# Performance work log

Hardware: AMD Instinct MI355X
Metric: run time of the kernel (lower is better)

Reference implementation:

```python
import jax, jax.numpy as jnp
import numpy as np

PATCH = 16

def setup_inputs() -> dict:
    key = jax.random.key(0)
    k1, k2, k3, k4, k5 = jax.random.split(key, 5)
    B, C, H, W = 128, 3, 224, 224
    N = (H // PATCH) * (W // PATCH)  # 196
    D = 768
    x = jax.random.normal(k1, (B, C, H, W), dtype=jnp.float32)
    ys = jax.random.randint(k2, (B, N), 0, H - PATCH + 1, dtype=jnp.int64)
    xs = jax.random.randint(k3, (B, N), 0, W - PATCH + 1, dtype=jnp.int64)
    W_proj = jax.random.normal(k4, (D, C * PATCH * PATCH), dtype=jnp.float32) * 0.02
    b_proj = jax.random.normal(k5, (D,), dtype=jnp.float32) * 0.02
    return {"x": x, "ys": ys, "xs": xs, "W_proj": W_proj, "b_proj": b_proj}

def reference(x, ys, xs, W_proj, b_proj):
    # x: [B, C, H, W]; ys, xs: [B, N] top-left patch coords
    B, C, H, W = x.shape
    N = ys.shape[1]
    P = PATCH
    # flattened within-patch offsets: d[p] = dy*W + dx, shape [P*P]
    dy = jnp.arange(P)[:, None]
    dx = jnp.arange(P)[None, :]
    d = (dy * W + dx).reshape(-1)  # [P*P]
    base = ys * W + xs                         # [B, N]
    indices = base[:, :, None] + d[None, None, :]  # [B, N, P*P]
    indices = indices.reshape(B, N * P * P)
    # gather over flattened spatial dims for every channel
    x_flat = x.reshape(B, C, H * W)
    patches = jnp.take_along_axis(
        x_flat, indices[:, None, :].astype(jnp.int32), axis=2
    )  # [B, C, N*P*P]
    patches = patches.reshape(B, C, N, P * P)
    patches = patches.transpose(0, 2, 1, 3).reshape(B, N, C * P * P)  # [B, N, C*P*P]
    patch_tokens = jnp.einsum('bnf,df->bnd', patches, W_proj) + b_proj  # [B, N, D]
    patch_positions = jnp.stack([ys, xs], axis=-1)  # [B, N, 2]
    return (patch_tokens, patch_positions)
```

## Files before the change

### kernel.cpp

```cpp
#include <hip/hip_runtime.h>
#include <hip/hip_bf16.h>

#define B_IMG   128
#define CH      3
#define HW      224
#define NPATCH  196
#define TOKENS  25088
#define PATCH   16
#define FDIM    768
#define DDIM    768
#define TOKELEMS ((size_t)TOKENS * FDIM)
#define OUT_TOKENS ((size_t)TOKENS * DDIM)

#define GATHER_BLOCKS (TOKENS * (FDIM / 4) / 256)
#define WCONV_BLOCKS  ((DDIM * FDIM / 4) / 256)

typedef short short8 __attribute__((ext_vector_type(8)));
typedef float f32x4  __attribute__((ext_vector_type(4)));

static __device__ __forceinline__ unsigned short f2bf(float v) {
  unsigned u = __float_as_uint(v);
  unsigned r = u + 0x7fffu + ((u >> 16) & 1u);
  return (unsigned short)(r >> 16);
}

static __device__ __forceinline__ void gload16(const short* g, short* l) {
  __builtin_amdgcn_global_load_lds(
      (const __attribute__((address_space(1))) void*)g,
      (__attribute__((address_space(3))) void*)l,
      16, 0, 0);
}

__global__ __launch_bounds__(256) void prep_kernel(
    const float* __restrict__ x, const int* __restrict__ ys,
    const int* __restrict__ xs, const float* __restrict__ W,
    short* __restrict__ patches, short* __restrict__ Wbf,
    float* __restrict__ pos) {
  const int blk = blockIdx.x;
  if (blk < GATHER_BLOCKS) {
    int e   = blk * 256 + threadIdx.x;
    int tok = e / 192;
    int q   = e - tok * 192;
    int f   = q * 4;
    int b   = tok / NPATCH;
    int y   = ys[tok];
    int xc  = xs[tok];
    int c   = f >> 8;
    int rem = f & 255;
    int py  = rem >> 4;
    int px  = rem & 15;
    const float* src = x + ((size_t)(b * CH + c) * HW + (y + py)) * HW + xc + px;
    ushort4 o;
    o.x = f2bf(src[0]); o.y = f2bf(src[1]); o.z = f2bf(src[2]); o.w = f2bf(src[3]);
    *(ushort4*)&patches[(size_t)tok * FDIM + f] = o;
    if (q == 0) {
      pos[(size_t)tok * 2]     = (float)y;
      pos[(size_t)tok * 2 + 1] = (float)xc;
    }
  } else {
    int i = ((blk - GATHER_BLOCKS) * 256 + threadIdx.x) * 4;
    float4 v = *(const float4*)&W[i];
    ushort4 o;
    o.x = f2bf(v.x); o.y = f2bf(v.y); o.z = f2bf(v.z); o.w = f2bf(v.w);
    *(ushort4*)&Wbf[i] = o;
  }
}

__global__ __launch_bounds__(256) void gemm_kernel(
    const short* __restrict__ A,
    const short* __restrict__ Bw,
    const float* __restrict__ bias,
    float* __restrict__ C) {
  __shared__ short At[4][128 * 32];
  __shared__ short Bt[4][128 * 32];

  const int tid  = threadIdx.x;
  const int w    = tid >> 6;
  const int l    = tid & 63;

  const int id  = blockIdx.x;
  const int nid = (id & 7) * 147 + (id >> 3);
  const int m0  = (nid / 6) * 128;
  const int n0  = (nid % 6) * 128;

  const int wrow = w >> 1;
  const int wcol = w & 1;
  const int lr   = l & 15;
  const int lg   = l >> 4;

  f32x4 acc[4][4];
  const f32x4 z = {0.f, 0.f, 0.f, 0.f};
#pragma unroll
  for (int mi = 0; mi < 4; ++mi)
#pragma unroll
    for (int ni = 0; ni < 4; ++ni) acc[mi][ni] = z;

  float bs[4];
#pragma unroll
  for (int ni = 0; ni < 4; ++ni)
    bs[ni] = bias[n0 + wcol * 64 + ni * 16 + lr];
#pragma unroll
  for (int ni = 0; ni < 4; ++ni) asm volatile("" : "+v"(bs[ni]));

  const int rw = w * 32;
  const short* gA = A + (size_t)(m0 + rw + (l >> 2)) * FDIM + ((l & 3) << 3);
  const short* gB = Bw + (size_t)(n0 + rw + (l >> 2)) * FDIM + ((l & 3) << 3);

  auto stage = [&](int buf, int kt) {
    const int ko = kt * 32;
    short* lA = &At[buf][rw * 32];
    short* lB = &Bt[buf][rw * 32];
    gload16(gA + ko, lA);
    gload16(gA + 16 * FDIM + ko, lA + 16 * 32);
    gload16(gB + ko, lB);
    gload16(gB + 16 * FDIM + ko, lB + 16 * 32);
  };
  auto compute = [&](int buf) {
    const short* Ab = At[buf];
    const short* Bb = Bt[buf];
    short8 a[4], b[4];
    const int koff = lg * 8;
#pragma unroll
    for (int mi = 0; mi < 4; ++mi)
      a[mi] = *(const short8*)&Ab[(wrow * 64 + mi * 16 + lr) * 32 + koff];
#pragma unroll
    for (int ni = 0; ni < 4; ++ni)
      b[ni] = *(const short8*)&Bb[(wcol * 64 + ni * 16 + lr) * 32 + koff];
    __builtin_amdgcn_s_setprio(1);
#pragma unroll
    for (int mi = 0; mi < 4; ++mi)
#pragma unroll
      for (int ni = 0; ni < 4; ++ni)
        acc[mi][ni] =
            __builtin_amdgcn_mfma_f32_16x16x32_bf16(a[mi], b[ni], acc[mi][ni], 0, 0, 0);
    __builtin_amdgcn_s_setprio(0);
  };

  stage(0, 0);
  stage(1, 1);
  stage(2, 2);

  for (int t = 0; t < 21; ++t) {
    stage((t + 3) & 3, t + 3);
    asm volatile("s_waitcnt vmcnt(12)" ::: "memory");
    __builtin_amdgcn_s_barrier();
    compute(t & 3);
    __builtin_amdgcn_s_barrier();
  }
  asm volatile("s_waitcnt vmcnt(8)" ::: "memory");
  __builtin_amdgcn_s_barrier();
  compute(21 & 3);
  __builtin_amdgcn_s_barrier();
  asm volatile("s_waitcnt vmcnt(4)" ::: "memory");
  __builtin_amdgcn_s_barrier();
  compute(22 & 3);
  __builtin_amdgcn_s_barrier();
  asm volatile("s_waitcnt vmcnt(0)" ::: "memory");
  __builtin_amdgcn_s_barrier();
  compute(23 & 3);

#pragma unroll
  for (int ni = 0; ni < 4; ++ni) {
    const int col = n0 + wcol * 64 + ni * 16 + lr;
#pragma unroll
    for (int mi = 0; mi < 4; ++mi) {
      const int row = m0 + wrow * 64 + mi * 16 + lg * 4;
      const f32x4 v = acc[mi][ni];
#pragma unroll
      for (int j = 0; j < 4; ++j)
        C[(size_t)(row + j) * DDIM + col] = v[j] + bs[ni];
    }
  }
}

__global__ __launch_bounds__(256) void naive_kernel(
    const float* __restrict__ x, const int* __restrict__ ys,
    const int* __restrict__ xs, const float* __restrict__ W,
    const float* __restrict__ bias, float* __restrict__ out) {
  __shared__ float prow[FDIM];
  const int tok = blockIdx.x;
  const int t   = threadIdx.x;
  const int b   = tok / NPATCH;
  const int y   = ys[tok];
  const int xc  = xs[tok];
  for (int i = t; i < FDIM; i += 256) {
    int c = i >> 8, rem = i & 255, py = rem >> 4, px = rem & 15;
    prow[i] = x[((size_t)(b * CH + c) * HW + y + py) * HW + xc + px];
  }
  __syncthreads();
  for (int dd = 0; dd < 3; ++dd) {
    const int d = t + dd * 256;
    float s = bias[d];
    const float4* wr = (const float4*)&W[(size_t)d * FDIM];
    const float4* pr = (const float4*)prow;
    for (int f4 = 0; f4 < FDIM / 4; ++f4) {
      float4 wv = wr[f4];
      float4 pv = pr[f4];
      s += wv.x * pv.x + wv.y * pv.y + wv.z * pv.z + wv.w * pv.w;
    }
    out[(size_t)tok * DDIM + d] = s;
  }
  if (t == 0) {
    float* pos = out + OUT_TOKENS;
    pos[(size_t)tok * 2]     = (float)y;
    pos[(size_t)tok * 2 + 1] = (float)xc;
  }
}

extern "C" void kernel_launch(void* const* d_in, const int* in_sizes, int n_in,
                              void* d_out, int out_size, void* d_ws, size_t ws_size,
                              hipStream_t stream) {
  const float* x    = (const float*)d_in[0];
  const int*   ys   = (const int*)d_in[1];
  const int*   xs   = (const int*)d_in[2];
  const float* W    = (const float*)d_in[3];
  const float* bias = (const float*)d_in[4];
  float* out = (float*)d_out;
  float* pos = out + OUT_TOKENS;

  const size_t w_bytes = (size_t)DDIM * FDIM * 2;
  const size_t p_bytes = TOKELEMS * 2;
  if (ws_size >= w_bytes + p_bytes) {
    short* Wbf     = (short*)d_ws;
    short* patches = (short*)d_ws + (size_t)DDIM * FDIM;
    prep_kernel<<<GATHER_BLOCKS + WCONV_BLOCKS, 256, 0, stream>>>(
        x, ys, xs, W, patches, Wbf, pos);
    gemm_kernel<<<(TOKENS / 128) * (DDIM / 128), 256, 0, stream>>>(
        patches, Wbf, bias, out);
  } else {
    naive_kernel<<<TOKENS, 256, 0, stream>>>(x, ys, xs, W, bias, out);
  }
}
```

Baseline: 89.94 us.

## Enlarge GEMM block tile to 256x128 with 8 waves sharing B tiles

Each GEMM block now holds a 256-row by 128-column output tile and runs 512 threads as 8 waves, so each staged B tile is reused by twice as many rows. The per-wave load split, the LDS buffers and the vmcnt wait counts are adjusted to match, and the XCD-aware block remapping is recomputed for the new count of 588 blocks. The goal is less global and L2 traffic for the weight operand. In exchange LDS per block grows to 96KB, which can limit how many blocks fit on a CU at once.

```diff
diff --git a/kernel.cpp b/kernel.cpp
--- a/kernel.cpp
+++ b/kernel.cpp
@@ -66,27 +66,30 @@
   }
 }
 
-__global__ __launch_bounds__(256) void gemm_kernel(
+__global__ __launch_bounds__(512) void gemm_kernel(
     const short* __restrict__ A,
     const short* __restrict__ Bw,
     const float* __restrict__ bias,
     float* __restrict__ C) {
-  __shared__ short At[4][128 * 32];
-  __shared__ short Bt[4][128 * 32];
-
-  const int tid  = threadIdx.x;
-  const int w    = tid >> 6;
-  const int l    = tid & 63;
-
-  const int id  = blockIdx.x;
-  const int nid = (id & 7) * 147 + (id >> 3);
-  const int m0  = (nid / 6) * 128;
-  const int n0  = (nid % 6) * 128;
-
-  const int wrow = w >> 1;
-  const int wcol = w & 1;
-  const int lr   = l & 15;
-  const int lg   = l >> 4;
+  __shared__ short As[4][256 * 32];
+  __shared__ short Bs[4][128 * 32];
+
+  const int tid = threadIdx.x;
+  const int w   = tid >> 6;
+  const int l   = tid & 63;
+  const int wr  = w >> 1;
+  const int wc  = w & 1;
+  const int lr  = l & 15;
+  const int lg  = l >> 4;
+
+  const int id   = blockIdx.x;
+  const int xcd  = id & 7;
+  const int chnk = id >> 3;
+  const int nid  = (xcd < 4 ? xcd * 74 : 4 * 74 + (xcd - 4) * 73) + chnk;
+  const int mt   = nid / 6;
+  const int nt   = nid - mt * 6;
+  const int m0   = mt * 256;
+  const int n0   = nt * 128;
 
   f32x4 acc[4][4];
   const f32x4 z = {0.f, 0.f, 0.f, 0.f};
@@ -98,34 +101,34 @@
   float bs[4];
 #pragma unroll
   for (int ni = 0; ni < 4; ++ni)
-    bs[ni] = bias[n0 + wcol * 64 + ni * 16 + lr];
+    bs[ni] = bias[n0 + wc * 64 + ni * 16 + lr];
 #pragma unroll
   for (int ni = 0; ni < 4; ++ni) asm volatile("" : "+v"(bs[ni]));
 
-  const int rw = w * 32;
-  const short* gA = A + (size_t)(m0 + rw + (l >> 2)) * FDIM + ((l & 3) << 3);
-  const short* gB = Bw + (size_t)(n0 + rw + (l >> 2)) * FDIM + ((l & 3) << 3);
-
-  auto stage = [&](int buf, int kt) {
-    const int ko = kt * 32;
-    short* lA = &At[buf][rw * 32];
-    short* lB = &Bt[buf][rw * 32];
+  const short* gA = A  + (size_t)(m0 + wr * 64 + wc * 32 + (l >> 2)) * FDIM + ((l & 3) << 3);
+  const short* gB = Bw + (size_t)(n0 + wc * 64 + wr * 16 + (l >> 2)) * FDIM + ((l & 3) << 3);
+  const int lAoff = (wr * 64 + wc * 32) * 32;
+  const int lBoff = (wc * 64 + wr * 16) * 32;
+
+  auto stage = [&](int slot, int s) {
+    const int ko = s * 32;
+    short* lA = &As[slot][lAoff];
+    short* lB = &Bs[slot][lBoff];
     gload16(gA + ko, lA);
     gload16(gA + 16 * FDIM + ko, lA + 16 * 32);
     gload16(gB + ko, lB);
-    gload16(gB + 16 * FDIM + ko, lB + 16 * 32);
   };
-  auto compute = [&](int buf) {
-    const short* Ab = At[buf];
-    const short* Bb = Bt[buf];
+  auto compute = [&](int slot) {
+    const short* Ab = As[slot];
+    const short* Bb = Bs[slot];
     short8 a[4], b[4];
     const int koff = lg * 8;
 #pragma unroll
     for (int mi = 0; mi < 4; ++mi)
-      a[mi] = *(const short8*)&Ab[(wrow * 64 + mi * 16 + lr) * 32 + koff];
+      a[mi] = *(const short8*)&Ab[(wr * 64 + mi * 16 + lr) * 32 + koff];
 #pragma unroll
     for (int ni = 0; ni < 4; ++ni)
-      b[ni] = *(const short8*)&Bb[(wcol * 64 + ni * 16 + lr) * 32 + koff];
+      b[ni] = *(const short8*)&Bb[(wc * 64 + ni * 16 + lr) * 32 + koff];
     __builtin_amdgcn_s_setprio(1);
 #pragma unroll
     for (int mi = 0; mi < 4; ++mi)
@@ -140,18 +143,18 @@
   stage(1, 1);
   stage(2, 2);
 
-  for (int t = 0; t < 21; ++t) {
-    stage((t + 3) & 3, t + 3);
-    asm volatile("s_waitcnt vmcnt(12)" ::: "memory");
+  for (int s = 0; s < 21; ++s) {
+    stage((s + 3) & 3, s + 3);
+    asm volatile("s_waitcnt vmcnt(9)" ::: "memory");
     __builtin_amdgcn_s_barrier();
-    compute(t & 3);
+    compute(s & 3);
     __builtin_amdgcn_s_barrier();
   }
-  asm volatile("s_waitcnt vmcnt(8)" ::: "memory");
+  asm volatile("s_waitcnt vmcnt(6)" ::: "memory");
   __builtin_amdgcn_s_barrier();
   compute(21 & 3);
   __builtin_amdgcn_s_barrier();
-  asm volatile("s_waitcnt vmcnt(4)" ::: "memory");
+  asm volatile("s_waitcnt vmcnt(3)" ::: "memory");
   __builtin_amdgcn_s_barrier();
   compute(22 & 3);
   __builtin_amdgcn_s_barrier();
@@ -161,10 +164,10 @@
 
 #pragma unroll
   for (int ni = 0; ni < 4; ++ni) {
-    const int col = n0 + wcol * 64 + ni * 16 + lr;
+    const int col = n0 + wc * 64 + ni * 16 + lr;
 #pragma unroll
     for (int mi = 0; mi < 4; ++mi) {
-      const int row = m0 + wrow * 64 + mi * 16 + lg * 4;
+      const int row = m0 + wr * 64 + mi * 16 + lg * 4;
       const f32x4 v = acc[mi][ni];
 #pragma unroll
       for (int j = 0; j < 4; ++j)
@@ -225,7 +228,7 @@
     short* patches = (short*)d_ws + (size_t)DDIM * FDIM;
     prep_kernel<<<GATHER_BLOCKS + WCONV_BLOCKS, 256, 0, stream>>>(
         x, ys, xs, W, patches, Wbf, pos);
-    gemm_kernel<<<(TOKENS / 128) * (DDIM / 128), 256, 0, stream>>>(
+    gemm_kernel<<<(TOKENS / 256) * (DDIM / 128), 512, 0, stream>>>(
         patches, Wbf, bias, out);
   } else {
     naive_kernel<<<TOKENS, 256, 0, stream>>>(x, ys, xs, W, bias, out);
```

After: 93.65 us. 1.04x slower.

## Use K=64 double-buffered LDS tiles with XOR swizzle in GEMM

Applied to the files above, without the earlier changes.

The GEMM mainloop moves from a 4-deep ring of K=32 tiles to a 2-deep double buffer of K=64 tiles, which halves the number of barrier pairs per block. Global-to-LDS loads and LDS reads now go through an XOR column swizzle that is meant to avoid LDS bank conflicts on the wider rows. Each compute step issues twice as many MFMAs per barrier. The trade-off is a shallower prefetch depth, which may expose more memory latency. LDS use stays at 64KB.

```diff
diff --git a/kernel.cpp b/kernel.cpp
--- a/kernel.cpp
+++ b/kernel.cpp
@@ -71,22 +71,28 @@
     const short* __restrict__ Bw,
     const float* __restrict__ bias,
     float* __restrict__ C) {
-  __shared__ short At[4][128 * 32];
-  __shared__ short Bt[4][128 * 32];
+  __shared__ short As[2][128 * 64];
+  __shared__ short Bs[2][128 * 64];
 
   const int tid  = threadIdx.x;
   const int w    = tid >> 6;
   const int l    = tid & 63;
+  const int wrow = w >> 1;
+  const int wcol = w & 1;
+  const int lr   = l & 15;
+  const int lg   = l >> 4;
 
   const int id  = blockIdx.x;
   const int nid = (id & 7) * 147 + (id >> 3);
   const int m0  = (nid / 6) * 128;
   const int n0  = (nid % 6) * 128;
 
-  const int wrow = w >> 1;
-  const int wcol = w & 1;
-  const int lr   = l & 15;
-  const int lg   = l >> 4;
+  float bs[4];
+#pragma unroll
+  for (int ni = 0; ni < 4; ++ni)
+    bs[ni] = bias[n0 + wcol * 64 + ni * 16 + lr];
+#pragma unroll
+  for (int ni = 0; ni < 4; ++ni) asm volatile("" : "+v"(bs[ni]));
 
   f32x4 acc[4][4];
   const f32x4 z = {0.f, 0.f, 0.f, 0.f};
@@ -95,69 +101,72 @@
 #pragma unroll
     for (int ni = 0; ni < 4; ++ni) acc[mi][ni] = z;
 
-  float bs[4];
-#pragma unroll
-  for (int ni = 0; ni < 4; ++ni)
-    bs[ni] = bias[n0 + wcol * 64 + ni * 16 + lr];
-#pragma unroll
-  for (int ni = 0; ni < 4; ++ni) asm volatile("" : "+v"(bs[ni]));
-
-  const int rw = w * 32;
-  const short* gA = A + (size_t)(m0 + rw + (l >> 2)) * FDIM + ((l & 3) << 3);
-  const short* gB = Bw + (size_t)(n0 + rw + (l >> 2)) * FDIM + ((l & 3) << 3);
-
-  auto stage = [&](int buf, int kt) {
-    const int ko = kt * 32;
-    short* lA = &At[buf][rw * 32];
-    short* lB = &Bt[buf][rw * 32];
-    gload16(gA + ko, lA);
-    gload16(gA + 16 * FDIM + ko, lA + 16 * 32);
-    gload16(gB + ko, lB);
-    gload16(gB + 16 * FDIM + ko, lB + 16 * 32);
-  };
-  auto compute = [&](int buf) {
-    const short* Ab = At[buf];
-    const short* Bb = Bt[buf];
-    short8 a[4], b[4];
-    const int koff = lg * 8;
-#pragma unroll
-    for (int mi = 0; mi < 4; ++mi)
-      a[mi] = *(const short8*)&Ab[(wrow * 64 + mi * 16 + lr) * 32 + koff];
-#pragma unroll
-    for (int ni = 0; ni < 4; ++ni)
-      b[ni] = *(const short8*)&Bb[(wcol * 64 + ni * 16 + lr) * 32 + koff];
-    __builtin_amdgcn_s_setprio(1);
-#pragma unroll
-    for (int mi = 0; mi < 4; ++mi)
-#pragma unroll
-      for (int ni = 0; ni < 4; ++ni)
-        acc[mi][ni] =
-            __builtin_amdgcn_mfma_f32_16x16x32_bf16(a[mi], b[ni], acc[mi][ni], 0, 0, 0);
-    __builtin_amdgcn_s_setprio(0);
-  };
-
-  stage(0, 0);
-  stage(1, 1);
-  stage(2, 2);
-
-  for (int t = 0; t < 21; ++t) {
-    stage((t + 3) & 3, t + 3);
-    asm volatile("s_waitcnt vmcnt(12)" ::: "memory");
+  const int srow = l >> 3;
+  const int scol = ((l & 7) ^ srow) * 8;
+  const short* gA = A  + (size_t)(m0 + w * 32 + srow) * FDIM + scol;
+  const short* gB = Bw + (size_t)(n0 + w * 32 + srow) * FDIM + scol;
+
+#define STAGE(BUF, KT)                                                     \
+  do {                                                                     \
+    const int ko_ = (KT) * 64;                                             \
+    _Pragma("unroll")                                                      \
+    for (int c_ = 0; c_ < 4; ++c_) {                                       \
+      gload16(gA + (size_t)c_ * 8 * FDIM + ko_,                            \
+              &As[(BUF)][(w * 32 + c_ * 8) * 64]);                         \
+      gload16(gB + (size_t)c_ * 8 * FDIM + ko_,                            \
+              &Bs[(BUF)][(w * 32 + c_ * 8) * 64]);                         \
+    }                                                                      \
+  } while (0)
+
+  const int rx  = lr & 7;
+  const int rd0 = ((0 + lg) ^ rx) * 8;
+  const int rd1 = ((4 + lg) ^ rx) * 8;
+
+#define COMPUTE(BUF)                                                       \
+  do {                                                                     \
+    const short* Ab_ = As[(BUF)];                                          \
+    const short* Bb_ = Bs[(BUF)];                                          \
+    short8 a0_[4], b0_[4], a1_[4], b1_[4];                                 \
+    _Pragma("unroll")                                                      \
+    for (int mi = 0; mi < 4; ++mi) {                                       \
+      const int r_ = (wrow * 64 + mi * 16 + lr) * 64;                      \
+      a0_[mi] = *(const short8*)&Ab_[r_ + rd0];                            \
+      a1_[mi] = *(const short8*)&Ab_[r_ + rd1];                            \
+    }                                                                      \
+    _Pragma("unroll")                                                      \
+    for (int ni = 0; ni < 4; ++ni) {                                       \
+      const int r_ = (wcol * 64 + ni * 16 + lr) * 64;                      \
+      b0_[ni] = *(const short8*)&Bb_[r_ + rd0];                            \
+      b1_[ni] = *(const short8*)&Bb_[r_ + rd1];                            \
+    }                                                                      \
+    __builtin_amdgcn_s_setprio(1);                                         \
+    _Pragma("unroll")                                                      \
+    for (int mi = 0; mi < 4; ++mi)                                         \
+      _Pragma("unroll")                                                    \
+      for (int ni = 0; ni < 4; ++ni) {                                     \
+        acc[mi][ni] = __builtin_amdgcn_mfma_f32_16x16x32_bf16(             \
+            a0_[mi], b0_[ni], acc[mi][ni], 0, 0, 0);                       \
+        acc[mi][ni] = __builtin_amdgcn_mfma_f32_16x16x32_bf16(             \
+            a1_[mi], b1_[ni], acc[mi][ni], 0, 0, 0);                       \
+      }                                                                    \
+    __builtin_amdgcn_s_setprio(0);                                         \
+  } while (0)
+
+  STAGE(0, 0);
+
+#pragma unroll 1
+  for (int s = 0; s < 11; ++s) {
+    STAGE((s + 1) & 1, s + 1);
+    asm volatile("s_waitcnt vmcnt(8)" ::: "memory");
     __builtin_amdgcn_s_barrier();
-    compute(t & 3);
+    COMPUTE(s & 1);
+    asm volatile("s_waitcnt lgkmcnt(0)" ::: "memory");
+    __builtin_amdgcn_sched_barrier(0);
     __builtin_amdgcn_s_barrier();
   }
-  asm volatile("s_waitcnt vmcnt(8)" ::: "memory");
-  __builtin_amdgcn_s_barrier();
-  compute(21 & 3);
-  __builtin_amdgcn_s_barrier();
-  asm volatile("s_waitcnt vmcnt(4)" ::: "memory");
-  __builtin_amdgcn_s_barrier();
-  compute(22 & 3);
-  __builtin_amdgcn_s_barrier();
   asm volatile("s_waitcnt vmcnt(0)" ::: "memory");
   __builtin_amdgcn_s_barrier();
-  compute(23 & 3);
+  COMPUTE(1);
 
 #pragma unroll
   for (int ni = 0; ni < 4; ++ni) {
@@ -171,6 +180,8 @@
         C[(size_t)(row + j) * DDIM + col] = v[j] + bs[ni];
     }
   }
+#undef STAGE
+#undef COMPUTE
 }
 
 __global__ __launch_bounds__(256) void naive_kernel(
```

Measured after the change: 86.26 us. 1.04x faster.
